# Kernel tuning notes

Hardware: AMD Instinct MI355X
Metric: run time of the kernel (lower is better)

## Reference

```python
import math
import jax, jax.numpy as jnp
import numpy as np

LMAX = 4
IN_FEATURES = 128
OUT_FEATURES = 128
BATCH = 16384
NUM_M = (LMAX + 1) ** 2  # 25


def setup_inputs() -> dict:
    key = jax.random.key(0)
    k1, k2 = jax.random.split(key)
    bound = 1.0 / math.sqrt(IN_FEATURES)
    input_embedding = jax.random.normal(k1, (BATCH, NUM_M, IN_FEATURES), dtype=jnp.float32)
    # Matches flax initializers.uniform(scale=2*bound): values in [0, 2*bound).
    # The module subtracts `bound` inside __call__, replicated in reference().
    weight = jax.random.uniform(k2, (LMAX + 1, OUT_FEATURES, IN_FEATURES),
                                dtype=jnp.float32, minval=0.0, maxval=2.0 * bound)
    bias = jnp.zeros((OUT_FEATURES,), dtype=jnp.float32)
    return {"input_embedding": input_embedding, "weight": weight, "bias": bias}


def reference(input_embedding, weight, bias):
    in_features = input_embedding.shape[-1]
    bound = 1.0 / math.sqrt(in_features)
    w = weight - bound  # centered weights, shape [lmax+1, out, in]
    lmax = weight.shape[0] - 1
    # expand_index[m] = l such that m lies in degree-l block (2l+1 entries each)
    expand_index = jnp.repeat(jnp.arange(lmax + 1), 2 * jnp.arange(lmax + 1) + 1,
                              total_repeat_length=(lmax + 1) ** 2)
    w_expanded = w[expand_index]  # [(lmax+1)^2, out, in] -- small gather
    out = jnp.einsum('bmi,moi->bmo', input_embedding, w_expanded)
    out = out.at[:, 0, :].add(bias)  # bias only on the l=0 (m=0) component
    return out
```

## Files before the change

### kernel.cpp

```cpp
#include <hip/hip_runtime.h>


#define BATCH 16384
#define NUM_M 25
#define NF 128
#define BB 64
#define ROWS_PER_BLOCK (BATCH / BB)
#define TILE_ROWS 64
#define NIT (ROWS_PER_BLOCK / TILE_ROWS)

typedef __attribute__((ext_vector_type(8))) short short8;
typedef __attribute__((ext_vector_type(4))) float floatx4;

__device__ inline short f2bf(float f) {
    union { float f; unsigned u; } v;
    v.f = f;
    unsigned r = v.u + 0x7fffu + ((v.u >> 16) & 1u);
    return (short)(r >> 16);
}

__device__ inline short8 cvt8(floatx4 x0, floatx4 x1) {
    short8 f;
    f[0] = f2bf(x0[0]); f[1] = f2bf(x0[1]);
    f[2] = f2bf(x0[2]); f[3] = f2bf(x0[3]);
    f[4] = f2bf(x1[0]); f[5] = f2bf(x1[1]);
    f[6] = f2bf(x1[2]); f[7] = f2bf(x1[3]);
    return f;
}

__global__ __launch_bounds__(256, 4)
void so3_mfma_kernel(const float* __restrict__ x,
                     const float* __restrict__ w,
                     const float* __restrict__ bias,
                     float* __restrict__ out) {
    __shared__ short wlds[NF * NF];

    const int m = blockIdx.y;
    const int l = (m >= 16) ? 4 : (m >= 9) ? 3 : (m >= 4) ? 2 : (m >= 1) ? 1 : 0;
    const int tid  = threadIdx.x;
    const int wave = tid >> 6;
    const int lane = tid & 63;
    const int q    = lane >> 4;
    const int n16  = lane & 15;
    const float bound = 0.08838834764831843f;

    const int b0   = blockIdx.x * ROWS_PER_BLOCK;
    const int row0 = b0 + wave * 16 + n16;
    const float* xr0 = x   + (row0 * NUM_M + m) * NF;
    float*       or0 = out + (row0 * NUM_M + m) * NF;
    const int tile_stride = TILE_ROWS * NUM_M * NF;

    floatx4 raw[8];
    #pragma unroll
    for (int kc = 0; kc < 4; ++kc) {
        const floatx4* p = (const floatx4*)(xr0 + kc * 32 + q * 8);
        raw[2 * kc]     = p[0];
        raw[2 * kc + 1] = p[1];
    }

    {
        const int o    = tid >> 1;
        const int half = tid & 1;
        const float* wr = w + l * NF * NF + o * NF + half * 64;
        char* wb = (char*)wlds;
        #pragma unroll
        for (int j = 0; j < 8; ++j) {
            floatx4 f0 = ((const floatx4*)wr)[2 * j];
            floatx4 f1 = ((const floatx4*)wr)[2 * j + 1];
            short8 s;
            s[0] = f2bf(f0[0] - bound); s[1] = f2bf(f0[1] - bound);
            s[2] = f2bf(f0[2] - bound); s[3] = f2bf(f0[3] - bound);
            s[4] = f2bf(f1[0] - bound); s[5] = f2bf(f1[1] - bound);
            s[6] = f2bf(f1[2] - bound); s[7] = f2bf(f1[3] - bound);
            const int c = half * 8 + j;
            *(short8*)(wb + o * 256 + ((c * 16) ^ ((o & 7) << 4))) = s;
        }
    }
    __syncthreads();

    const char* wb = (const char*)wlds;
    const int xm = (n16 & 7) << 4;
    int lr[4];
    #pragma unroll
    for (int kc = 0; kc < 4; ++kc)
        lr[kc] = n16 * 256 + ((kc * 64 + q * 16) ^ xm);

    short8 afrag[4];
    #pragma unroll
    for (int kc = 0; kc < 4; ++kc)
        afrag[kc] = cvt8(raw[2 * kc], raw[2 * kc + 1]);

    #pragma unroll
    for (int it = 0; it < NIT; ++it) {
        if (it + 1 < NIT) {
            const float* xr = xr0 + (it + 1) * tile_stride;
            #pragma unroll
            for (int kc = 0; kc < 4; ++kc) {
                const floatx4* p = (const floatx4*)(xr + kc * 32 + q * 8);
                raw[2 * kc]     = p[0];
                raw[2 * kc + 1] = p[1];
            }
        }

        floatx4 acc[8] = {};
        #pragma unroll
        for (int kc = 0; kc < 4; ++kc) {
            short8 wt[8];
            #pragma unroll
            for (int nt = 0; nt < 8; ++nt)
                wt[nt] = *(const short8*)(wb + lr[kc] + nt * 4096);
            #pragma unroll
            for (int nt = 0; nt < 8; ++nt)
                acc[nt] = __builtin_amdgcn_mfma_f32_16x16x32_bf16(
                    wt[nt], afrag[kc], acc[nt], 0, 0, 0);
        }

        float* orow = or0 + it * tile_stride;
        #pragma unroll
        for (int nt = 0; nt < 8; ++nt) {
            floatx4 v = acc[nt];
            if (m == 0) {
                const floatx4 b4 = *(const floatx4*)(bias + nt * 16 + q * 4);
                v[0] += b4[0]; v[1] += b4[1]; v[2] += b4[2]; v[3] += b4[3];
            }
            __builtin_nontemporal_store(v, (floatx4*)(orow + nt * 16 + q * 4));
        }

        if (it + 1 < NIT) {
            #pragma unroll
            for (int kc = 0; kc < 4; ++kc)
                afrag[kc] = cvt8(raw[2 * kc], raw[2 * kc + 1]);
        }
    }
}

extern "C" void kernel_launch(void* const* d_in, const int* in_sizes, int n_in,
                              void* d_out, int out_size, void* d_ws, size_t ws_size,
                              hipStream_t stream) {
    const float* x    = (const float*)d_in[0];
    const float* w    = (const float*)d_in[1];
    const float* bias = (const float*)d_in[2];
    float* out = (float*)d_out;

    dim3 grid(BB, NUM_M);
    dim3 block(256);
    so3_mfma_kernel<<<grid, block, 0, stream>>>(x, w, bias, out);
}
```

Baseline: 396.1 us.

## Stage input and output tiles through LDS for row-contiguous coalesced global access

```diff
diff --git a/kernel.cpp b/kernel.cpp
--- a/kernel.cpp
+++ b/kernel.cpp
@@ -10,6 +10,7 @@
 #define NIT (ROWS_PER_BLOCK / TILE_ROWS)
 
 typedef __attribute__((ext_vector_type(8))) short short8;
+typedef __attribute__((ext_vector_type(4))) short bf16x4;
 typedef __attribute__((ext_vector_type(4))) float floatx4;
 
 __device__ inline short f2bf(float f) {
@@ -19,118 +20,131 @@
     return (short)(r >> 16);
 }
 
-__device__ inline short8 cvt8(floatx4 x0, floatx4 x1) {
-    short8 f;
-    f[0] = f2bf(x0[0]); f[1] = f2bf(x0[1]);
-    f[2] = f2bf(x0[2]); f[3] = f2bf(x0[3]);
-    f[4] = f2bf(x1[0]); f[5] = f2bf(x1[1]);
-    f[6] = f2bf(x1[2]); f[7] = f2bf(x1[3]);
-    return f;
-}
-
-__global__ __launch_bounds__(256, 4)
+__global__ __launch_bounds__(256, 2)
 void so3_mfma_kernel(const float* __restrict__ x,
                      const float* __restrict__ w,
                      const float* __restrict__ bias,
                      float* __restrict__ out) {
     __shared__ short wlds[NF * NF];
+    __shared__ short xlds[TILE_ROWS * NF];
+    __shared__ float olds[TILE_ROWS * NF];
 
     const int m = blockIdx.y;
     const int l = (m >= 16) ? 4 : (m >= 9) ? 3 : (m >= 4) ? 2 : (m >= 1) ? 1 : 0;
     const int tid  = threadIdx.x;
+    const int lane = tid & 63;
     const int wave = tid >> 6;
-    const int lane = tid & 63;
     const int q    = lane >> 4;
     const int n16  = lane & 15;
+    const int hw   = tid >> 5;
+    const int j    = tid & 31;
     const float bound = 0.08838834764831843f;
-
-    const int b0   = blockIdx.x * ROWS_PER_BLOCK;
-    const int row0 = b0 + wave * 16 + n16;
-    const float* xr0 = x   + (row0 * NUM_M + m) * NF;
-    float*       or0 = out + (row0 * NUM_M + m) * NF;
-    const int tile_stride = TILE_ROWS * NUM_M * NF;
+    const int b0 = blockIdx.x * ROWS_PER_BLOCK;
 
     floatx4 raw[8];
     #pragma unroll
-    for (int kc = 0; kc < 4; ++kc) {
-        const floatx4* p = (const floatx4*)(xr0 + kc * 32 + q * 8);
-        raw[2 * kc]     = p[0];
-        raw[2 * kc + 1] = p[1];
+    for (int k = 0; k < 8; ++k) {
+        const int r = b0 + hw * 8 + k;
+        raw[k] = *(const floatx4*)(x + (r * NUM_M + m) * NF + j * 4);
     }
+    __builtin_amdgcn_sched_barrier(0);
 
     {
         const int o    = tid >> 1;
         const int half = tid & 1;
         const float* wr = w + l * NF * NF + o * NF + half * 64;
-        char* wb = (char*)wlds;
+        char* wbp = (char*)wlds;
         #pragma unroll
-        for (int j = 0; j < 8; ++j) {
-            floatx4 f0 = ((const floatx4*)wr)[2 * j];
-            floatx4 f1 = ((const floatx4*)wr)[2 * j + 1];
+        for (int jj = 0; jj < 8; ++jj) {
+            floatx4 f0 = ((const floatx4*)wr)[2 * jj];
+            floatx4 f1 = ((const floatx4*)wr)[2 * jj + 1];
             short8 s;
             s[0] = f2bf(f0[0] - bound); s[1] = f2bf(f0[1] - bound);
             s[2] = f2bf(f0[2] - bound); s[3] = f2bf(f0[3] - bound);
             s[4] = f2bf(f1[0] - bound); s[5] = f2bf(f1[1] - bound);
             s[6] = f2bf(f1[2] - bound); s[7] = f2bf(f1[3] - bound);
-            const int c = half * 8 + j;
-            *(short8*)(wb + o * 256 + ((c * 16) ^ ((o & 7) << 4))) = s;
+            const int c = half * 8 + jj;
+            *(short8*)(wbp + o * 256 + ((c * 16) ^ ((o & 7) << 4))) = s;
+        }
+    }
+    {
+        char* xbp = (char*)xlds;
+        #pragma unroll
+        for (int k = 0; k < 8; ++k) {
+            bf16x4 s;
+            s[0] = f2bf(raw[k][0]); s[1] = f2bf(raw[k][1]);
+            s[2] = f2bf(raw[k][2]); s[3] = f2bf(raw[k][3]);
+            const int r = hw * 8 + k;
+            *(bf16x4*)(xbp + r * 256 + ((j * 8) ^ (k << 4))) = s;
         }
     }
     __syncthreads();
 
-    const char* wb = (const char*)wlds;
+    const char* wbp = (const char*)wlds;
+    const char* xbp = (const char*)xlds;
+    char* obp = (char*)olds;
     const int xm = (n16 & 7) << 4;
     int lr[4];
     #pragma unroll
     for (int kc = 0; kc < 4; ++kc)
         lr[kc] = n16 * 256 + ((kc * 64 + q * 16) ^ xm);
 
-    short8 afrag[4];
-    #pragma unroll
-    for (int kc = 0; kc < 4; ++kc)
-        afrag[kc] = cvt8(raw[2 * kc], raw[2 * kc + 1]);
+    floatx4 bval = {0.0f, 0.0f, 0.0f, 0.0f};
+    if (m == 0) bval = *(const floatx4*)(bias + j * 4);
 
-    #pragma unroll
     for (int it = 0; it < NIT; ++it) {
         if (it + 1 < NIT) {
-            const float* xr = xr0 + (it + 1) * tile_stride;
             #pragma unroll
-            for (int kc = 0; kc < 4; ++kc) {
-                const floatx4* p = (const floatx4*)(xr + kc * 32 + q * 8);
-                raw[2 * kc]     = p[0];
-                raw[2 * kc + 1] = p[1];
+            for (int k = 0; k < 8; ++k) {
+                const int r = b0 + (it + 1) * TILE_ROWS + hw * 8 + k;
+                raw[k] = *(const floatx4*)(x + (r * NUM_M + m) * NF + j * 4);
             }
+            __builtin_amdgcn_sched_barrier(0);
         }
 
         floatx4 acc[8] = {};
         #pragma unroll
         for (int kc = 0; kc < 4; ++kc) {
+            const short8 a = *(const short8*)(xbp + wave * 4096 + lr[kc]);
             short8 wt[8];
             #pragma unroll
             for (int nt = 0; nt < 8; ++nt)
-                wt[nt] = *(const short8*)(wb + lr[kc] + nt * 4096);
+                wt[nt] = *(const short8*)(wbp + lr[kc] + nt * 4096);
             #pragma unroll
             for (int nt = 0; nt < 8; ++nt)
                 acc[nt] = __builtin_amdgcn_mfma_f32_16x16x32_bf16(
-                    wt[nt], afrag[kc], acc[nt], 0, 0, 0);
+                    wt[nt], a, acc[nt], 0, 0, 0);
         }
 
-        float* orow = or0 + it * tile_stride;
+        const int orow = (wave * 16 + n16) * 512;
         #pragma unroll
-        for (int nt = 0; nt < 8; ++nt) {
-            floatx4 v = acc[nt];
-            if (m == 0) {
-                const floatx4 b4 = *(const floatx4*)(bias + nt * 16 + q * 4);
-                v[0] += b4[0]; v[1] += b4[1]; v[2] += b4[2]; v[3] += b4[3];
-            }
-            __builtin_nontemporal_store(v, (floatx4*)(orow + nt * 16 + q * 4));
-        }
+        for (int nt = 0; nt < 8; ++nt)
+            *(floatx4*)(obp + orow + ((nt * 64 + q * 16) ^ xm)) = acc[nt];
+
+        __syncthreads();
 
         if (it + 1 < NIT) {
             #pragma unroll
-            for (int kc = 0; kc < 4; ++kc)
-                afrag[kc] = cvt8(raw[2 * kc], raw[2 * kc + 1]);
+            for (int k = 0; k < 8; ++k) {
+                bf16x4 s;
+                s[0] = f2bf(raw[k][0]); s[1] = f2bf(raw[k][1]);
+                s[2] = f2bf(raw[k][2]); s[3] = f2bf(raw[k][3]);
+                const int r = hw * 8 + k;
+                *(bf16x4*)((char*)xlds + r * 256 + ((j * 8) ^ (k << 4))) = s;
+            }
         }
+
+        #pragma unroll
+        for (int k = 0; k < 8; ++k) {
+            const int rloc = hw * 8 + k;
+            floatx4 v = *(const floatx4*)(obp + rloc * 512 + ((j * 16) ^ (k << 4)));
+            v[0] += bval[0]; v[1] += bval[1]; v[2] += bval[2]; v[3] += bval[3];
+            const int r = b0 + it * TILE_ROWS + rloc;
+            __builtin_nontemporal_store(
+                v, (floatx4*)(out + (r * NUM_M + m) * NF + j * 4));
+        }
+
+        __syncthreads();
     }
 }
 
```

Measured after the change: 373.0 us. 5.8% less time.

## Group blocks by degree l so each block's M rows share one weight matrix

Applied to the files above, without the earlier changes.

```diff
diff --git a/kernel.cpp b/kernel.cpp
--- a/kernel.cpp
+++ b/kernel.cpp
@@ -1,13 +1,9 @@
 #include <hip/hip_runtime.h>
 
 
-#define BATCH 16384
+#define NF 128
 #define NUM_M 25
-#define NF 128
-#define BB 64
-#define ROWS_PER_BLOCK (BATCH / BB)
-#define TILE_ROWS 64
-#define NIT (ROWS_PER_BLOCK / TILE_ROWS)
+#define ROWSTRIDE (NUM_M * NF)
 
 typedef __attribute__((ext_vector_type(8))) short short8;
 typedef __attribute__((ext_vector_type(4))) float floatx4;
@@ -19,24 +15,31 @@
     return (short)(r >> 16);
 }
 
-__device__ inline short8 cvt8(floatx4 x0, floatx4 x1) {
-    short8 f;
-    f[0] = f2bf(x0[0]); f[1] = f2bf(x0[1]);
-    f[2] = f2bf(x0[2]); f[3] = f2bf(x0[3]);
-    f[4] = f2bf(x1[0]); f[5] = f2bf(x1[1]);
-    f[6] = f2bf(x1[2]); f[7] = f2bf(x1[3]);
-    return f;
+template<int L>
+__device__ __forceinline__ void issue_tile(const float* __restrict__ x,
+                                           int tile, int n16, int q,
+                                           floatx4 (&raw)[8], int& rowoff) {
+    constexpr int G  = 2 * L + 1;
+    constexpr int M0 = L * L;
+    const int bm = tile * 16 + n16;
+    const int b  = bm / G;
+    const int r  = bm - b * G;
+    rowoff = b * ROWSTRIDE + (M0 + r) * NF;
+    const float* xp = x + rowoff + q * 8;
+    #pragma unroll
+    for (int kc = 0; kc < 4; ++kc) {
+        raw[2 * kc]     = *(const floatx4*)(xp + kc * 32);
+        raw[2 * kc + 1] = *(const floatx4*)(xp + kc * 32 + 4);
+    }
 }
 
-__global__ __launch_bounds__(256, 4)
-void so3_mfma_kernel(const float* __restrict__ x,
-                     const float* __restrict__ w,
-                     const float* __restrict__ bias,
-                     float* __restrict__ out) {
-    __shared__ short wlds[NF * NF];
-
-    const int m = blockIdx.y;
-    const int l = (m >= 16) ? 4 : (m >= 9) ? 3 : (m >= 4) ? 2 : (m >= 1) ? 1 : 0;
+template<int L>
+__device__ __forceinline__ void so3_run(int lblk,
+                                        const float* __restrict__ x,
+                                        const float* __restrict__ w,
+                                        const float* __restrict__ bias,
+                                        float* __restrict__ out,
+                                        short* wlds, float* blds) {
     const int tid  = threadIdx.x;
     const int wave = tid >> 6;
     const int lane = tid & 63;
@@ -44,62 +47,61 @@
     const int n16  = lane & 15;
     const float bound = 0.08838834764831843f;
 
-    const int b0   = blockIdx.x * ROWS_PER_BLOCK;
-    const int row0 = b0 + wave * 16 + n16;
-    const float* xr0 = x   + (row0 * NUM_M + m) * NF;
-    float*       or0 = out + (row0 * NUM_M + m) * NF;
-    const int tile_stride = TILE_ROWS * NUM_M * NF;
+    const int tbase = lblk * 16 + wave * 4;
 
-    floatx4 raw[8];
-    #pragma unroll
-    for (int kc = 0; kc < 4; ++kc) {
-        const floatx4* p = (const floatx4*)(xr0 + kc * 32 + q * 8);
-        raw[2 * kc]     = p[0];
-        raw[2 * kc + 1] = p[1];
-    }
+    floatx4 rawA[8], rawB[8];
+    int offA = 0, offB = 0;
+    issue_tile<L>(x, tbase + 0, n16, q, rawA, offA);
+    __builtin_amdgcn_sched_barrier(0);
 
     {
         const int o    = tid >> 1;
         const int half = tid & 1;
-        const float* wr = w + l * NF * NF + o * NF + half * 64;
-        char* wb = (char*)wlds;
+        const float* wr = w + L * NF * NF + o * NF + half * 64;
+        char* wbp = (char*)wlds;
         #pragma unroll
-        for (int j = 0; j < 8; ++j) {
-            floatx4 f0 = ((const floatx4*)wr)[2 * j];
-            floatx4 f1 = ((const floatx4*)wr)[2 * j + 1];
+        for (int jj = 0; jj < 8; ++jj) {
+            floatx4 f0 = ((const floatx4*)wr)[2 * jj];
+            floatx4 f1 = ((const floatx4*)wr)[2 * jj + 1];
             short8 s;
             s[0] = f2bf(f0[0] - bound); s[1] = f2bf(f0[1] - bound);
             s[2] = f2bf(f0[2] - bound); s[3] = f2bf(f0[3] - bound);
             s[4] = f2bf(f1[0] - bound); s[5] = f2bf(f1[1] - bound);
             s[6] = f2bf(f1[2] - bound); s[7] = f2bf(f1[3] - bound);
-            const int c = half * 8 + j;
-            *(short8*)(wb + o * 256 + ((c * 16) ^ ((o & 7) << 4))) = s;
+            const int c = half * 8 + jj;
+            *(short8*)(wbp + o * 256 + ((c * 16) ^ ((o & 15) << 4))) = s;
         }
+        if (L == 0 && tid < NF) blds[tid] = bias[tid];
     }
     __syncthreads();
 
-    const char* wb = (const char*)wlds;
-    const int xm = (n16 & 7) << 4;
+    const char* wbp = (const char*)wlds;
     int lr[4];
     #pragma unroll
     for (int kc = 0; kc < 4; ++kc)
-        lr[kc] = n16 * 256 + ((kc * 64 + q * 16) ^ xm);
-
-    short8 afrag[4];
-    #pragma unroll
-    for (int kc = 0; kc < 4; ++kc)
-        afrag[kc] = cvt8(raw[2 * kc], raw[2 * kc + 1]);
+        lr[kc] = n16 * 256 + ((kc * 64 + q * 16) ^ (n16 << 4));
 
     #pragma unroll
-    for (int it = 0; it < NIT; ++it) {
-        if (it + 1 < NIT) {
-            const float* xr = xr0 + (it + 1) * tile_stride;
-            #pragma unroll
-            for (int kc = 0; kc < 4; ++kc) {
-                const floatx4* p = (const floatx4*)(xr + kc * 32 + q * 8);
-                raw[2 * kc]     = p[0];
-                raw[2 * kc + 1] = p[1];
-            }
+    for (int t = 0; t < 4; ++t) {
+        floatx4* cur = (t & 1) ? rawB : rawA;
+        const int rowoff = (t & 1) ? offB : offA;
+
+        if (t < 3) {
+            if (t & 1) issue_tile<L>(x, tbase + t + 1, n16, q, rawA, offA);
+            else       issue_tile<L>(x, tbase + t + 1, n16, q, rawB, offB);
+            __builtin_amdgcn_sched_barrier(0);
+        }
+
+        short8 afrag[4];
+        #pragma unroll
+        for (int kc = 0; kc < 4; ++kc) {
+            floatx4 x0 = cur[2 * kc], x1 = cur[2 * kc + 1];
+            short8 f;
+            f[0] = f2bf(x0[0]); f[1] = f2bf(x0[1]);
+            f[2] = f2bf(x0[2]); f[3] = f2bf(x0[3]);
+            f[4] = f2bf(x1[0]); f[5] = f2bf(x1[1]);
+            f[6] = f2bf(x1[2]); f[7] = f2bf(x1[3]);
+            afrag[kc] = f;
         }
 
         floatx4 acc[8] = {};
@@ -108,30 +110,39 @@
             short8 wt[8];
             #pragma unroll
             for (int nt = 0; nt < 8; ++nt)
-                wt[nt] = *(const short8*)(wb + lr[kc] + nt * 4096);
+                wt[nt] = *(const short8*)(wbp + lr[kc] + nt * 4096);
             #pragma unroll
             for (int nt = 0; nt < 8; ++nt)
                 acc[nt] = __builtin_amdgcn_mfma_f32_16x16x32_bf16(
                     wt[nt], afrag[kc], acc[nt], 0, 0, 0);
         }
 
-        float* orow = or0 + it * tile_stride;
+        float* op = out + rowoff + q * 4;
         #pragma unroll
         for (int nt = 0; nt < 8; ++nt) {
             floatx4 v = acc[nt];
-            if (m == 0) {
-                const floatx4 b4 = *(const floatx4*)(bias + nt * 16 + q * 4);
-                v[0] += b4[0]; v[1] += b4[1]; v[2] += b4[2]; v[3] += b4[3];
+            if (L == 0) {
+                const floatx4 bv = *(const floatx4*)(blds + nt * 16 + q * 4);
+                v[0] += bv[0]; v[1] += bv[1]; v[2] += bv[2]; v[3] += bv[3];
             }
-            __builtin_nontemporal_store(v, (floatx4*)(orow + nt * 16 + q * 4));
-        }
-
-        if (it + 1 < NIT) {
-            #pragma unroll
-            for (int kc = 0; kc < 4; ++kc)
-                afrag[kc] = cvt8(raw[2 * kc], raw[2 * kc + 1]);
+            __builtin_nontemporal_store(v, (floatx4*)(op + nt * 16));
         }
     }
+}
+
+__global__ __launch_bounds__(256, 3)
+void so3_kernel(const float* __restrict__ x,
+                const float* __restrict__ w,
+                const float* __restrict__ bias,
+                float* __restrict__ out) {
+    __shared__ short wlds[NF * NF];
+    __shared__ float blds[NF];
+    const int bx = blockIdx.x;
+    if      (bx <   64) so3_run<0>(bx,        x, w, bias, out, wlds, blds);
+    else if (bx <  256) so3_run<1>(bx -   64, x, w, bias, out, wlds, blds);
+    else if (bx <  576) so3_run<2>(bx -  256, x, w, bias, out, wlds, blds);
+    else if (bx < 1024) so3_run<3>(bx -  576, x, w, bias, out, wlds, blds);
+    else                so3_run<4>(bx - 1024, x, w, bias, out, wlds, blds);
 }
 
 extern "C" void kernel_launch(void* const* d_in, const int* in_sizes, int n_in,
@@ -142,7 +153,7 @@
     const float* bias = (const float*)d_in[2];
     float* out = (float*)d_out;
 
-    dim3 grid(BB, NUM_M);
+    dim3 grid(1600);
     dim3 block(256);
-    so3_mfma_kernel<<<grid, block, 0, stream>>>(x, w, bias, out);
+    so3_kernel<<<grid, block, 0, stream>>>(x, w, bias, out);
 }
```

After: 397.6 us. No clear change (+0.4%).
